# Kernel optimization log

Measured on AMD Instinct MI355X. Metric: run time of the kernel, lower is better.

Reference implementation:

```python
import jax, jax.numpy as jnp
import numpy as np

T, B, I, H, E = 32, 128, 64, 128, 4
N_TRAP = 100  # trapezoid intervals -> 101 sample points


def setup_inputs() -> dict:
    key = jax.random.key(0)
    ks = jax.random.split(key, 14)
    s_cell = 1.0 / np.sqrt(I + H)
    s_wh = 1.0 / np.sqrt((I + H) * E)

    def u(k, shape, s):
        return jax.random.uniform(k, shape, jnp.float32, -s, s)

    return {
        "x_time": jax.random.normal(ks[0], (T, B, I), jnp.float32),
        "dt_time": jax.random.uniform(ks[1], (T, B), jnp.float32, 0.01, 1.0),
        "Wh_w": u(ks[2], ((I + H) * E, H * E), s_wh),
        "Wh_b": u(ks[3], (H * E,), s_wh),
        "Wi_w": u(ks[4], (E, I + H, H), s_cell),
        "Wi_b": u(ks[5], (E, H), s_cell),
        "Wf_w": u(ks[6], (E, I + H, H), s_cell),
        "Wf_b": u(ks[7], (E, H), s_cell),
        "Wd_w": u(ks[8], (E, I + H, H), s_cell),
        "Wd_b": u(ks[9], (E, H), s_cell),
        "Wg_w": u(ks[10], (E, I + H, H), s_cell),
        "Wg_b": u(ks[11], (E, H), s_cell),
        "Wo_w": u(ks[12], (E, I + H, H), s_cell),
        "Wo_b": u(ks[13], (E, H), s_cell),
        "alpha": jnp.ones((E, H), jnp.float32) / H,
    }


def reference(x_time, dt_time, Wh_w, Wh_b, Wi_w, Wi_b, Wf_w, Wf_b,
              Wd_w, Wd_b, Wg_w, Wg_b, Wo_w, Wo_b, alpha):
    t_total, batch, in_dim = x_time.shape
    e_types, hid = alpha.shape
    ts_unit = jnp.linspace(0.0, 1.0, N_TRAP + 1, dtype=x_time.dtype)  # [101]

    def step(carry, inp):
        h, c = carry            # each [E,B,H]
        x, dt = inp             # [B,I], [B]
        # hidden_sum = Wh(cat_m([x, h_m]))
        cat = jnp.concatenate(
            [jnp.concatenate([x, h[m]], axis=-1) for m in range(e_types)], axis=-1)  # [B,(I+H)*E]
        hs = (cat @ Wh_w + Wh_b).reshape(batch, e_types, hid).transpose(1, 0, 2)     # [E,B,H]
        iv = jnp.concatenate(
            [jnp.broadcast_to(x[None], (e_types, batch, in_dim)), hs], axis=-1)       # [E,B,I+H]

        def gate(W, b):
            return jnp.einsum('ebd,edh->ebh', iv, W) + b[:, None, :]

        i_g = jax.nn.sigmoid(gate(Wi_w, Wi_b))
        f_g = jax.nn.sigmoid(gate(Wf_w, Wf_b))
        g = f_g * c + i_g * jnp.tanh(gate(Wg_w, Wg_b))   # curr_g
        delta = jnp.exp(gate(Wd_w, Wd_b))                 # curr_delta
        o = jax.nn.sigmoid(gate(Wo_w, Wo_b))              # curr_o
        diff = c - g                                      # prev_c - curr_g

        c_new = g + diff * jnp.exp(-delta * dt[None, :, None])  # c_t at dt
        h_new = o * jnp.tanh(c_new)
        lam = jnp.einsum('eh,ebh->eb', alpha, h_new)             # intensity at dt

        # trapezoidal integration of intensity over [0, dt], 100 intervals
        ts = dt[:, None] * ts_unit                                # [B,101]
        cv = g[:, :, None, :] + diff[:, :, None, :] * jnp.exp(
            -delta[:, :, None, :] * ts[None, :, :, None])         # [E,B,101,H]
        fv = jnp.einsum('eh,ebth->ebt', alpha, o[:, :, None, :] * jnp.tanh(cv))  # [E,B,101]
        integ = (dt[None, :] / N_TRAP) * (
            jnp.sum(fv, axis=-1) - 0.5 * (fv[..., 0] + fv[..., -1]))  # [E,B]

        return (h_new, c_new), (lam.T, integ.T)  # outputs [B,E]

    h0 = jnp.zeros((e_types, batch, hid), x_time.dtype)
    c0 = jnp.zeros_like(h0)
    _, (lambdas, lambda_integrals) = jax.lax.scan(step, (h0, c0), (x_time, dt_time))
    return lambdas, lambda_integrals  # each [T,B,E]
```

## Files before the change

### kernel.cpp

```cpp
#include <hip/hip_runtime.h>

#define OFF_WALL   0
#define OFF_BIAS   196608
#define OFF_WHHH   199680
#define OFF_WGH    330752
#define OFF_XG     494592
#define OFF_GST    13077504
#define OFF_HBUF   21466112

typedef _Float16 half2_t __attribute__((ext_vector_type(2)));

__device__ __forceinline__ float fast_sig(float x) {
    return __fdividef(1.f, 1.f + __expf(-x));
}
__device__ __forceinline__ float sig_e(float y) {
    return __builtin_amdgcn_rcpf(__expf(y) + 1.f);
}
__device__ __forceinline__ unsigned pack2h(float a, float b) {
    _Float16 ha = (_Float16)a, hb = (_Float16)b;
    unsigned short ua = __builtin_bit_cast(unsigned short, ha);
    unsigned short ub = __builtin_bit_cast(unsigned short, hb);
    return ((unsigned)ub << 16) | ua;
}
__device__ __forceinline__ float dot2(unsigned w, unsigned h, float acc) {
    return __builtin_amdgcn_fdot2(__builtin_bit_cast(half2_t, w),
                                  __builtin_bit_cast(half2_t, h), acc, false);
}

__global__ __launch_bounds__(256) void k0_pack(
    const float* __restrict__ Wh_w, const float* __restrict__ Wh_b,
    const float* __restrict__ Wi_w, const float* __restrict__ Wi_b,
    const float* __restrict__ Wf_w, const float* __restrict__ Wf_b,
    const float* __restrict__ Wd_w, const float* __restrict__ Wd_b,
    const float* __restrict__ Wg_w, const float* __restrict__ Wg_b,
    const float* __restrict__ Wo_w, const float* __restrict__ Wo_b,
    float* __restrict__ ws)
{
    const float* gw[5] = {Wi_w, Wf_w, Wd_w, Wg_w, Wo_w};
    const float* gb[5] = {Wi_b, Wf_b, Wd_b, Wg_b, Wo_b};
    int idx = blockIdx.x * 256 + threadIdx.x;
    if (idx < 196608) {
        int r = idx / 3072, col = idx - r * 3072;
        float v;
        if (col < 512) {
            v = Wh_w[r * 512 + col] + Wh_w[(192 + r) * 512 + col]
              + Wh_w[(384 + r) * 512 + col] + Wh_w[(576 + r) * 512 + col];
        } else {
            int q = col - 512;
            int e = q / 640;
            int rem = q - e * 640;
            int g = rem >> 7, h = rem & 127;
            v = gw[g][(e * 192 + r) * 128 + h];
        }
        ws[OFF_WALL + idx] = v;
    } else if (idx < 327680) {
        int i = idx - 196608;
        int q    = i & 3;
        int lane = (i >> 2) & 127;
        int i4   = (i >> 9) & 15;
        int kq   = (i >> 13) & 3;
        int e    = i >> 15;
        int kp = i4 * 4 + q;
        int k0 = kq * 128 + 2 * kp;
        int r0 = (k0 >> 7) * 192 + 64 + (k0 & 127);
        float w0 = Wh_w[r0 * 512 + e * 128 + lane];
        float w1 = Wh_w[(r0 + 1) * 512 + e * 128 + lane];
        reinterpret_cast<unsigned*>(ws + OFF_WHHH)[i] = pack2h(w0, w1);
    } else if (idx < 491520) {
        int i = idx - 327680;
        int lane = i & 127;
        int gg = (i >> 7) % 5;
        int rest = (i >> 7) / 5;
        int ii = rest & 15;
        int kq = (rest >> 4) & 3;
        int e  = rest >> 6;
        int k0 = kq * 32 + 2 * ii, k1 = k0 + 1;
        float w0 = gw[gg][(e * 192 + 64 + k0) * 128 + lane];
        float w1 = gw[gg][(e * 192 + 64 + k1) * 128 + lane];
        reinterpret_cast<unsigned*>(ws + OFF_WGH)[i] = pack2h(w0, w1);
    }
    if (idx < 3072) {
        float v;
        if (idx < 512) v = Wh_b[idx];
        else {
            int q = idx - 512;
            int e = q / 640;
            int rem = q - e * 640;
            int g = rem >> 7, h = rem & 127;
            v = gb[g][e * 128 + h];
        }
        ws[OFF_BIAS + idx] = v;
    }
    if (idx < 262144) {
        reinterpret_cast<unsigned*>(ws + OFF_HBUF)[idx] = 0xFFFFFFFFu;
    }
}

__global__ __launch_bounds__(256) void k1_xproj(
    const float* __restrict__ x, const float* wsr, float* XG)
{
    __shared__ __align__(16) float XT[64 * 68];
    const float* W_all = wsr + OFF_WALL;
    const float* bias  = wsr + OFF_BIAS;
    int bid = blockIdx.x;
    int ct = bid % 48, rt = bid / 48;
    int r0 = rt * 64, c0 = ct * 64;
    for (int p = threadIdx.x; p < 4096; p += 256) {
        int i = p >> 6, k = p & 63;
        XT[k * 68 + i] = x[(r0 + i) * 64 + k];
    }
    __syncthreads();
    int col = c0 + (threadIdx.x & 63);
    int iq = threadIdx.x >> 6;
    float acc[16];
    #pragma unroll
    for (int r = 0; r < 16; r++) acc[r] = 0.f;
    const float* wp = W_all + col;
    #pragma unroll 4
    for (int k = 0; k < 64; k++) {
        float w = wp[k * 3072];
        const float4* xt4 = reinterpret_cast<const float4*>(&XT[k * 68 + iq * 16]);
        #pragma unroll
        for (int r4 = 0; r4 < 4; r4++) {
            float4 xv = xt4[r4];
            acc[r4 * 4 + 0] = fmaf(xv.x, w, acc[r4 * 4 + 0]);
            acc[r4 * 4 + 1] = fmaf(xv.y, w, acc[r4 * 4 + 1]);
            acc[r4 * 4 + 2] = fmaf(xv.z, w, acc[r4 * 4 + 2]);
            acc[r4 * 4 + 3] = fmaf(xv.w, w, acc[r4 * 4 + 3]);
        }
    }
    float bv = bias[col];
    #pragma unroll
    for (int r = 0; r < 16; r++) {
        int row = r0 + iq * 16 + r;
        XG[row * 3072 + col] = acc[r] + bv;
    }
}

__global__ __launch_bounds__(512, 1) void k2_recur(
    const uint4* __restrict__ WhhH4,
    const unsigned* __restrict__ WgH,
    const float* __restrict__ XG,
    const float* __restrict__ dt_time,
    const float* __restrict__ alpha,
    float4* __restrict__ Gst4,
    unsigned* __restrict__ hbuf,
    float* __restrict__ lam_out)
{
    __shared__ __align__(16) uint4 waL[8192];
    __shared__ __align__(16) unsigned hsP[2][64];
    __shared__ __align__(16) unsigned hOut[128];
    __shared__ float pA[4][2][128];
    __shared__ float pB[4][2][5][128];
    __shared__ float red[4];
    const int tid = threadIdx.x;
    const int bid = blockIdx.x;
    const int e   = (bid >> 3) & 3;
    const int grp = (bid & 7) | ((bid >> 5) << 3);
    const int b0  = grp * 2;
    const int kq  = tid >> 7;
    const int lane = tid & 127;
    const int l64 = tid & 63;
    const int s = (tid >> 7) & 1, l = lane;

    {
        const uint4* src = WhhH4 + (size_t)e * 8192;
        #pragma unroll
        for (int n = 0; n < 16; ++n) waL[tid + 512 * n] = src[tid + 512 * n];
    }
    unsigned wg[5][16];
    #pragma unroll
    for (int i = 0; i < 16; i++) {
        #pragma unroll
        for (int g = 0; g < 5; g++)
            wg[g][i] = WgH[(((e * 4 + kq) * 16 + i) * 5 + g) * 128 + lane];
    }
    const float av = alpha[e * 128 + lane];
    float cst = 0.f;
    __syncthreads();

    for (int t = 0; t < 32; ++t) {
        const int row0 = t * 128 + b0;
        float xg0 = 0.f, xgg0 = 0.f, xgg1 = 0.f, xgg2 = 0.f, xgg3 = 0.f, xgg4 = 0.f;
        if (tid < 256) {
            const float* base = XG + (size_t)(row0 + s) * 3072;
            xg0 = base[e * 128 + l];
            const float* gp = base + 512 + e * 640 + l;
            xgg0 = gp[0]; xgg1 = gp[128]; xgg2 = gp[256]; xgg3 = gp[384]; xgg4 = gp[512];
        }
        if (t > 0) {
            uint2 hu;
            if (kq == e) {
                hu.x = hOut[l64];
                hu.y = hOut[64 + l64];
            } else {
                const unsigned long long* ap =
                    reinterpret_cast<const unsigned long long*>(
                        hbuf + ((size_t)((t & 1) * 64 + grp) * 4 + e) * 512)
                    + (kq * 64 + l64);
                unsigned long long v = __hip_atomic_load(ap, __ATOMIC_RELAXED,
                                                         __HIP_MEMORY_SCOPE_AGENT);
                while ((unsigned)v == 0xFFFFFFFFu ||
                       (unsigned)(v >> 32) == 0xFFFFFFFFu) {
                    __builtin_amdgcn_s_sleep(1);
                    v = __hip_atomic_load(ap, __ATOMIC_RELAXED,
                                          __HIP_MEMORY_SCOPE_AGENT);
                }
                hu.x = (unsigned)v;
                hu.y = (unsigned)(v >> 32);
            }
            float a0 = 0.f, a1 = 0.f;
            #pragma unroll
            for (int i4 = 0; i4 < 16; ++i4) {
                uint4 w = waL[(kq * 16 + i4) * 128 + lane];
                unsigned h0, h1;
                h0 = __builtin_amdgcn_readlane(hu.x, i4 * 4 + 0);
                h1 = __builtin_amdgcn_readlane(hu.y, i4 * 4 + 0);
                a0 = dot2(w.x, h0, a0); a1 = dot2(w.x, h1, a1);
                h0 = __builtin_amdgcn_readlane(hu.x, i4 * 4 + 1);
                h1 = __builtin_amdgcn_readlane(hu.y, i4 * 4 + 1);
                a0 = dot2(w.y, h0, a0); a1 = dot2(w.y, h1, a1);
                h0 = __builtin_amdgcn_readlane(hu.x, i4 * 4 + 2);
                h1 = __builtin_amdgcn_readlane(hu.y, i4 * 4 + 2);
                a0 = dot2(w.z, h0, a0); a1 = dot2(w.z, h1, a1);
                h0 = __builtin_amdgcn_readlane(hu.x, i4 * 4 + 3);
                h1 = __builtin_amdgcn_readlane(hu.y, i4 * 4 + 3);
                a0 = dot2(w.w, h0, a0); a1 = dot2(w.w, h1, a1);
            }
            pA[kq][0][lane] = a0;
            pA[kq][1][lane] = a1;
        }
        __syncthreads();
        if (t > 0 && kq != e && lane < 64) {
            unsigned long long* ap =
                reinterpret_cast<unsigned long long*>(
                    hbuf + ((size_t)((t & 1) * 64 + grp) * 4 + e) * 512)
                + (kq * 64 + l64);
            __hip_atomic_store(ap, ~0ull, __ATOMIC_RELAXED, __HIP_MEMORY_SCOPE_AGENT);
        }
        if (tid < 256) {
            float hs = xg0;
            if (t > 0) hs += pA[0][s][l] + pA[1][s][l] + pA[2][s][l] + pA[3][s][l];
            float hi = __shfl_down(hs, 1, 64);
            if ((l & 1) == 0) hsP[s][l >> 1] = pack2h(hs, hi);
        }
        __syncthreads();
        float b0a = 0.f, b1a = 0.f, b2a = 0.f, b3a = 0.f, b4a = 0.f;
        float b0b = 0.f, b1b = 0.f, b2b = 0.f, b3b = 0.f, b4b = 0.f;
        {
            unsigned hv = hsP[(l64 >> 4) & 1][kq * 16 + (l64 & 15)];
            #pragma unroll
            for (int i = 0; i < 16; ++i) {
                unsigned h0 = __builtin_amdgcn_readlane(hv, i);
                unsigned h1 = __builtin_amdgcn_readlane(hv, 16 + i);
                b0a = dot2(wg[0][i], h0, b0a); b0b = dot2(wg[0][i], h1, b0b);
                b1a = dot2(wg[1][i], h0, b1a); b1b = dot2(wg[1][i], h1, b1b);
                b2a = dot2(wg[2][i], h0, b2a); b2b = dot2(wg[2][i], h1, b2b);
                b3a = dot2(wg[3][i], h0, b3a); b3b = dot2(wg[3][i], h1, b3b);
                b4a = dot2(wg[4][i], h0, b4a); b4b = dot2(wg[4][i], h1, b4b);
            }
        }
        pB[kq][0][0][lane] = b0a; pB[kq][0][1][lane] = b1a; pB[kq][0][2][lane] = b2a;
        pB[kq][0][3][lane] = b3a; pB[kq][0][4][lane] = b4a;
        pB[kq][1][0][lane] = b0b; pB[kq][1][1][lane] = b1b; pB[kq][1][2][lane] = b2b;
        pB[kq][1][3][lane] = b3b; pB[kq][1][4][lane] = b4b;
        __syncthreads();
        if (tid < 256) {
            float ai = pB[0][s][0][l] + pB[1][s][0][l] + pB[2][s][0][l] + pB[3][s][0][l] + xgg0;
            float af = pB[0][s][1][l] + pB[1][s][1][l] + pB[2][s][1][l] + pB[3][s][1][l] + xgg1;
            float ad = pB[0][s][2][l] + pB[1][s][2][l] + pB[2][s][2][l] + pB[3][s][2][l] + xgg2;
            float ag = pB[0][s][3][l] + pB[1][s][3][l] + pB[2][s][3][l] + pB[3][s][3][l] + xgg3;
            float ao = pB[0][s][4][l] + pB[1][s][4][l] + pB[2][s][4][l] + pB[3][s][4][l] + xgg4;
            float ig = fast_sig(ai);
            float fg = fast_sig(af);
            float dl = __expf(ad);
            float gt = tanhf(ag);
            float og = fast_sig(ao);
            float gc = fmaf(fg, cst, ig * gt);
            float df = cst - gc;
            float dtv = dt_time[row0 + s];
            cst = fmaf(df, __expf(-dl * dtv), gc);
            float hn = og * tanhf(cst);
            float4 stv;
            stv.x = 2.f * gc; stv.y = 2.f * df; stv.z = dl * dtv; stv.w = av * og;
            Gst4[(size_t)(row0 + s) * 512 + e * 128 + l] = stv;
            float hi = __shfl_down(hn, 1, 64);
            if ((l & 1) == 0) {
                unsigned pw = pack2h(hn, hi);
                hOut[s * 64 + (l >> 1)] = pw;
                const int wi = (e * 64 + (l >> 1)) * 2 + s;
                unsigned* basep = hbuf + (size_t)(((t + 1) & 1) * 64 + grp) * 4 * 512;
                #pragma unroll
                for (int c = 0; c < 4; ++c) {
                    if (c != e) {
                        __hip_atomic_store(basep + (size_t)c * 512 + wi, pw,
                                           __ATOMIC_RELAXED, __HIP_MEMORY_SCOPE_AGENT);
                    }
                }
            }
            float lm = av * hn;
            #pragma unroll
            for (int off = 32; off > 0; off >>= 1) lm += __shfl_down(lm, off, 64);
            if ((tid & 63) == 0) red[tid >> 6] = lm;
        }
        __syncthreads();
        if (tid == 0) {
            lam_out[(row0 + 0) * 4 + e] = red[0] + red[1];
            lam_out[(row0 + 1) * 4 + e] = red[2] + red[3];
        }
    }
}

__global__ __launch_bounds__(256) void k3_trap(
    const float4* __restrict__ Gst4, const float* __restrict__ dt_time,
    float* __restrict__ integ_out)
{
    __shared__ float red[4];
    const int bidx = blockIdx.x;
    const int row = bidx >> 2;
    const int e   = bidx & 3;
    const int tid = threadIdx.x;
    const int l   = tid & 127;
    const int half = tid >> 7;
    const float dtv = dt_time[row];
    float4 stv = Gst4[(size_t)row * 512 + e * 128 + l];
    float g2 = stv.x, d2 = stv.y, q = stv.z, ao = stv.w;
    float r  = __expf(-0.01f * q);
    float r2 = r * r, r4 = r2 * r2;
    float T;
    if (half == 0) {
        float E1 = r, E2 = r2, E3 = r2 * r, E4 = r4;
        float s1 = 0.f, s2 = 0.f, s3 = 0.f, s4 = 0.f;
        #pragma unroll
        for (int k = 0; k < 12; ++k) {
            s1 += sig_e(fmaf(d2, E1, g2)); E1 *= r4;
            s2 += sig_e(fmaf(d2, E2, g2)); E2 *= r4;
            s3 += sig_e(fmaf(d2, E3, g2)); E3 *= r4;
            s4 += sig_e(fmaf(d2, E4, g2)); E4 *= r4;
        }
        T = 48.5f - 2.f * ((s1 + s2) + (s3 + s4)) - sig_e(g2 + d2);
    } else {
        float E49 = __expf(-0.49f * q);
        float E1 = E49, E2 = E49 * r, E3 = E49 * r2, E4 = E49 * r2 * r;
        float s1 = 0.f, s2 = 0.f, s3 = 0.f, s4 = 0.f;
        #pragma unroll
        for (int k = 0; k < 13; ++k) {
            s1 += sig_e(fmaf(d2, E1, g2)); E1 *= r4;
            s2 += sig_e(fmaf(d2, E2, g2)); E2 *= r4;
            s3 += sig_e(fmaf(d2, E3, g2)); E3 *= r4;
            s4 += sig_e(fmaf(d2, E4, g2)); E4 *= r4;
        }
        float e100 = __expf(-q);
        T = 51.5f - 2.f * ((s1 + s2) + (s3 + s4)) + sig_e(fmaf(d2, e100, g2));
    }
    float v = ao * T;
    #pragma unroll
    for (int off = 32; off > 0; off >>= 1) v += __shfl_down(v, off, 64);
    if ((tid & 63) == 0) red[tid >> 6] = v;
    __syncthreads();
    if (tid == 0) {
        float vv = (red[0] + red[1]) + (red[2] + red[3]);
        integ_out[row * 4 + e] = vv * (dtv * 0.01f);
    }
}

extern "C" void kernel_launch(void* const* d_in, const int* in_sizes, int n_in,
                              void* d_out, int out_size, void* d_ws, size_t ws_size,
                              hipStream_t stream)
{
    const float* x_time  = (const float*)d_in[0];
    const float* dt_time = (const float*)d_in[1];
    const float* Wh_w = (const float*)d_in[2];
    const float* Wh_b = (const float*)d_in[3];
    const float* Wi_w = (const float*)d_in[4];
    const float* Wi_b = (const float*)d_in[5];
    const float* Wf_w = (const float*)d_in[6];
    const float* Wf_b = (const float*)d_in[7];
    const float* Wd_w = (const float*)d_in[8];
    const float* Wd_b = (const float*)d_in[9];
    const float* Wg_w = (const float*)d_in[10];
    const float* Wg_b = (const float*)d_in[11];
    const float* Wo_w = (const float*)d_in[12];
    const float* Wo_b = (const float*)d_in[13];
    const float* alpha = (const float*)d_in[14];

    float* ws = (float*)d_ws;
    float* XG   = ws + OFF_XG;
    float4* Gst4 = (float4*)(ws + OFF_GST);
    unsigned* hbuf = (unsigned*)(ws + OFF_HBUF);
    float* lam_out   = (float*)d_out;
    float* integ_out = lam_out + 32 * 128 * 4;

    k0_pack<<<1920, 256, 0, stream>>>(Wh_w, Wh_b, Wi_w, Wi_b, Wf_w, Wf_b,
                                      Wd_w, Wd_b, Wg_w, Wg_b, Wo_w, Wo_b, ws);
    k1_xproj<<<3072, 256, 0, stream>>>(x_time, ws, XG);
    k2_recur<<<256, 512, 0, stream>>>(
        (const uint4*)(ws + OFF_WHHH), (const unsigned*)(ws + OFF_WGH),
        XG, dt_time, alpha, Gst4, hbuf, lam_out);
    k3_trap<<<16384, 256, 0, stream>>>(Gst4, dt_time, integ_out);
}
```

Before: 205.0 us.

## Move lambda reduction from recurrent kernel into trap kernel, batch units per block

The recurrent kernel no longer does the per-step warp reduction and extra barrier for lambda. Instead it writes alpha*h into a spare slot of the XG buffer, and the trap kernel reduces it. The trap kernel now processes 8 (row, expert) units per block with fewer blocks. It also pairs sigmoids to share one reciprocal and clamps exponent inputs. The aim is to shorten the serial critical path of the recurrence, at the cost of extra global writes and a looped trap kernel with two barriers per unit.

```diff
diff --git a/kernel.cpp b/kernel.cpp
--- a/kernel.cpp
+++ b/kernel.cpp
@@ -140,19 +140,17 @@
 __global__ __launch_bounds__(512, 1) void k2_recur(
     const uint4* __restrict__ WhhH4,
     const unsigned* __restrict__ WgH,
-    const float* __restrict__ XG,
+    float* __restrict__ XG,
     const float* __restrict__ dt_time,
     const float* __restrict__ alpha,
     float4* __restrict__ Gst4,
-    unsigned* __restrict__ hbuf,
-    float* __restrict__ lam_out)
+    unsigned* __restrict__ hbuf)
 {
     __shared__ __align__(16) uint4 waL[8192];
     __shared__ __align__(16) unsigned hsP[2][64];
     __shared__ __align__(16) unsigned hOut[128];
     __shared__ float pA[4][2][128];
     __shared__ float pB[4][2][5][128];
-    __shared__ float red[4];
     const int tid = threadIdx.x;
     const int bid = blockIdx.x;
     const int e   = (bid >> 3) & 3;
@@ -284,6 +282,7 @@
             float4 stv;
             stv.x = 2.f * gc; stv.y = 2.f * df; stv.z = dl * dtv; stv.w = av * og;
             Gst4[(size_t)(row0 + s) * 512 + e * 128 + l] = stv;
+            XG[(size_t)(row0 + s) * 3072 + 512 + e * 640 + l] = av * hn;
             float hi = __shfl_down(hn, 1, 64);
             if ((l & 1) == 0) {
                 unsigned pw = pack2h(hn, hi);
@@ -298,69 +297,80 @@
                     }
                 }
             }
-            float lm = av * hn;
-            #pragma unroll
-            for (int off = 32; off > 0; off >>= 1) lm += __shfl_down(lm, off, 64);
-            if ((tid & 63) == 0) red[tid >> 6] = lm;
-        }
-        __syncthreads();
-        if (tid == 0) {
-            lam_out[(row0 + 0) * 4 + e] = red[0] + red[1];
-            lam_out[(row0 + 1) * 4 + e] = red[2] + red[3];
-        }
+        }
+        __syncthreads();
     }
 }
 
 __global__ __launch_bounds__(256) void k3_trap(
-    const float4* __restrict__ Gst4, const float* __restrict__ dt_time,
-    float* __restrict__ integ_out)
+    const float4* __restrict__ Gst4, const float* __restrict__ XG,
+    const float* __restrict__ dt_time,
+    float* __restrict__ lam_out, float* __restrict__ integ_out)
 {
     __shared__ float red[4];
-    const int bidx = blockIdx.x;
-    const int row = bidx >> 2;
-    const int e   = bidx & 3;
+    __shared__ float redL[2];
     const int tid = threadIdx.x;
     const int l   = tid & 127;
     const int half = tid >> 7;
-    const float dtv = dt_time[row];
-    float4 stv = Gst4[(size_t)row * 512 + e * 128 + l];
-    float g2 = stv.x, d2 = stv.y, q = stv.z, ao = stv.w;
-    float r  = __expf(-0.01f * q);
-    float r2 = r * r, r4 = r2 * r2;
-    float T;
-    if (half == 0) {
-        float E1 = r, E2 = r2, E3 = r2 * r, E4 = r4;
+    #pragma unroll 1
+    for (int u = 0; u < 8; ++u) {
+        const int unit = blockIdx.x * 8 + u;
+        const int row = unit >> 2;
+        const int e   = unit & 3;
+        const float dtv = dt_time[row];
+        float4 stv = Gst4[(size_t)row * 512 + e * 128 + l];
+        float g2 = stv.x, d2 = stv.y, q = stv.z, ao = stv.w;
+        float avhn = 0.f;
+        if (half == 0) avhn = XG[(size_t)row * 3072 + 512 + e * 640 + l];
+        float r  = __expf(-0.01f * q);
+        float r2 = r * r, r4 = r2 * r2;
+        float T;
+        float E1, E2, E3, E4;
+        int iters;
+        float Tb;
+        if (half == 0) {
+            E1 = r; E2 = r2; E3 = r2 * r; E4 = r4;
+            iters = 12;
+            Tb = 48.5f - sig_e(fminf(g2 + d2, 60.f));
+        } else {
+            float E49 = __expf(-0.49f * q);
+            E1 = E49; E2 = E49 * r; E3 = E49 * r2; E4 = E49 * r2 * r;
+            iters = 13;
+            float e100 = __expf(-q);
+            Tb = 51.5f + sig_e(fminf(fmaf(d2, e100, g2), 60.f));
+        }
         float s1 = 0.f, s2 = 0.f, s3 = 0.f, s4 = 0.f;
+        for (int k = 0; k < iters; ++k) {
+            float y1 = fminf(fmaf(d2, E1, g2), 60.f);
+            float y2 = fminf(fmaf(d2, E2, g2), 60.f);
+            float y3 = fminf(fmaf(d2, E3, g2), 60.f);
+            float y4 = fminf(fmaf(d2, E4, g2), 60.f);
+            float B1 = __expf(y1) + 1.f, B2 = __expf(y2) + 1.f;
+            float B3 = __expf(y3) + 1.f, B4 = __expf(y4) + 1.f;
+            float ra = __builtin_amdgcn_rcpf(B1 * B2);
+            float rb = __builtin_amdgcn_rcpf(B3 * B4);
+            s1 = fmaf(ra, B2, s1); s2 = fmaf(ra, B1, s2);
+            s3 = fmaf(rb, B4, s3); s4 = fmaf(rb, B3, s4);
+            E1 *= r4; E2 *= r4; E3 *= r4; E4 *= r4;
+        }
+        T = Tb - 2.f * ((s1 + s2) + (s3 + s4));
+        float v = ao * T;
         #pragma unroll
-        for (int k = 0; k < 12; ++k) {
-            s1 += sig_e(fmaf(d2, E1, g2)); E1 *= r4;
-            s2 += sig_e(fmaf(d2, E2, g2)); E2 *= r4;
-            s3 += sig_e(fmaf(d2, E3, g2)); E3 *= r4;
-            s4 += sig_e(fmaf(d2, E4, g2)); E4 *= r4;
-        }
-        T = 48.5f - 2.f * ((s1 + s2) + (s3 + s4)) - sig_e(g2 + d2);
-    } else {
-        float E49 = __expf(-0.49f * q);
-        float E1 = E49, E2 = E49 * r, E3 = E49 * r2, E4 = E49 * r2 * r;
-        float s1 = 0.f, s2 = 0.f, s3 = 0.f, s4 = 0.f;
-        #pragma unroll
-        for (int k = 0; k < 13; ++k) {
-            s1 += sig_e(fmaf(d2, E1, g2)); E1 *= r4;
-            s2 += sig_e(fmaf(d2, E2, g2)); E2 *= r4;
-            s3 += sig_e(fmaf(d2, E3, g2)); E3 *= r4;
-            s4 += sig_e(fmaf(d2, E4, g2)); E4 *= r4;
-        }
-        float e100 = __expf(-q);
-        T = 51.5f - 2.f * ((s1 + s2) + (s3 + s4)) + sig_e(fmaf(d2, e100, g2));
-    }
-    float v = ao * T;
-    #pragma unroll
-    for (int off = 32; off > 0; off >>= 1) v += __shfl_down(v, off, 64);
-    if ((tid & 63) == 0) red[tid >> 6] = v;
-    __syncthreads();
-    if (tid == 0) {
-        float vv = (red[0] + red[1]) + (red[2] + red[3]);
-        integ_out[row * 4 + e] = vv * (dtv * 0.01f);
+        for (int off = 32; off > 0; off >>= 1) v += __shfl_down(v, off, 64);
+        if ((tid & 63) == 0) red[tid >> 6] = v;
+        if (half == 0) {
+            float lv = avhn;
+            #pragma unroll
+            for (int off = 32; off > 0; off >>= 1) lv += __shfl_down(lv, off, 64);
+            if ((tid & 63) == 0) redL[tid >> 6] = lv;
+        }
+        __syncthreads();
+        if (tid == 0) {
+            integ_out[row * 4 + e] =
+                ((red[0] + red[1]) + (red[2] + red[3])) * (dtv * 0.01f);
+            lam_out[row * 4 + e] = redL[0] + redL[1];
+        }
+        __syncthreads();
     }
 }
 
@@ -396,6 +406,6 @@
     k1_xproj<<<3072, 256, 0, stream>>>(x_time, ws, XG);
     k2_recur<<<256, 512, 0, stream>>>(
         (const uint4*)(ws + OFF_WHHH), (const unsigned*)(ws + OFF_WGH),
-        XG, dt_time, alpha, Gst4, hbuf, lam_out);
-    k3_trap<<<16384, 256, 0, stream>>>(Gst4, dt_time, integ_out);
-}
+        XG, dt_time, alpha, Gst4, hbuf);
+    k3_trap<<<2048, 256, 0, stream>>>(Gst4, XG, dt_time, lam_out, integ_out);
+}
```

Result: slower. 209.6 us (+2.3%).
